# Kernel tuning notes

Measured on AMD Instinct MI355X. Metric: run time of the kernel, lower is better.

## Reference

```python
import jax, jax.numpy as jnp
import numpy as np
from jax import lax

H = 64
V = 32000
B = 32
T = 512


def setup_inputs() -> dict:
    key = jax.random.key(0)
    k1, k2, k3, k4 = jax.random.split(key, 4)
    # Parameters, constructed exactly as in SOHMM.__init__
    alpha_exp = jax.nn.softmax(jax.random.normal(k1, (H, H, H), dtype=jnp.float32), axis=2)
    beta = jax.nn.log_softmax(jax.random.normal(k2, (H, V), dtype=jnp.float32), axis=1)
    gamma = jax.nn.log_softmax(jax.random.normal(k3, (H, H), dtype=jnp.float32).reshape(-1)).reshape(H, H)
    input_ids = jax.random.randint(k4, (B, T), 0, V, dtype=jnp.int64)
    return {"alpha_exp": alpha_exp, "beta": beta, "gamma": gamma, "input_ids": input_ids}


def reference(alpha_exp, beta, gamma, input_ids):
    # input_ids: [B, T]
    h = alpha_exp.shape[0]
    b, t = input_ids.shape
    ids = input_ids.T  # [T, B]
    mask = (ids != -1)
    # emission log-probs per timestep: [T, H, B]; -1 padding tokens zeroed
    ip = jnp.transpose(beta[:, jnp.where(mask, ids, 0)], (1, 0, 2)) * mask[:, None, :].astype(beta.dtype)
    gamma_exp = jax.nn.softmax(gamma.reshape(-1)).reshape(gamma.shape)

    # t = T-1: y starts at zeros then adds emission
    y0 = jnp.zeros((h, h, b), dtype=beta.dtype) + ip[-1][None, :, :]

    def step(y, ip_t):
        y_max = y.max(axis=(0, 1), keepdims=True)            # [1,1,B]
        y_exp = jnp.exp(y - y_max)
        y = jnp.log(jnp.einsum('ijk,jkb->ijb', alpha_exp, y_exp)) + y_max
        y = y + ip_t[None, :, :]
        return y, y

    # loop t = T-2 .. 0 (reverse over remaining emissions)
    y_last, ys_rest = lax.scan(step, y0, ip[:-1][::-1])
    ys = jnp.concatenate([y0[None], ys_rest], axis=0)       # [T, H, H, B]

    y_max = y_last.max(axis=(0, 1))                          # [B]
    final = jnp.log(jnp.einsum('ij,ijb->b', gamma_exp, jnp.exp(y_last - y_max[None, None, :]))) + y_max
    return ys, final
```

## Files before the change

kernel.cpp:

```cpp
#include <hip/hip_runtime.h>
#include <cstdint>
#include <cstddef>

#define Hh 64
#define Vv 32000
#define Bb 32
#define Tt 512

typedef _Float16 half2_t __attribute__((ext_vector_type(2)));

#define IP_OFF    0ull
#define IP_SZ     ((size_t)Bb*Tt*Hh*4)
#define SL_OFF    (IP_OFF + IP_SZ)
#define SL_SZ     ((size_t)Bb*Tt*4)
#define U511_OFF  (SL_OFF + SL_SZ)
#define U511_SZ   ((size_t)Bb*Hh*Hh*4)
#define STAGE_OFF (U511_OFF + U511_SZ)
#define STAGE_SZ  ((size_t)Tt*Bb*Hh*Hh*2)

__device__ __forceinline__ float wave_max64(float v){
  #pragma unroll
  for (int off=32; off; off>>=1) v = fmaxf(v, __shfl_xor(v, off, 64));
  return v;
}

__device__ __forceinline__ half2_t pk16(float x, float y){
  return __builtin_bit_cast(half2_t, __builtin_amdgcn_cvt_pkrtz(x, y));
}

__global__ __launch_bounds__(256) void sohmm_ipfill(
    const float* __restrict__ beta, const int* __restrict__ ids,
    float* __restrict__ ipbuf)
{
  const int bid = blockIdx.x;
  const int b = bid >> 7, tq = bid & 127;
  const int t = tq*4 + (threadIdx.x >> 6);
  const int j = threadIdx.x & 63;
  const int id = ids[b*Tt + t];
  ipbuf[((size_t)b*Tt + t)*Hh + j] = beta[(size_t)j*Vv + id];
}

__global__ __launch_bounds__(512)
__attribute__((amdgpu_waves_per_eu(2, 2)))
void sohmm_scan(
    const float* __restrict__ alpha, const float* __restrict__ ipbuf,
    float* __restrict__ out, float* __restrict__ SL,
    float* __restrict__ u511, unsigned int* __restrict__ stage, int use_stage)
{
  const int b    = blockIdx.x;
  const int tid  = threadIdx.x;
  const int j    = tid >> 3;
  const int igrp = tid & 7;
  const int w    = tid >> 6;
  const int lane = tid & 63;
  const int i0   = igrp * 8;

  __shared__ char zb[2][64*128];
  __shared__ char aL[512*272];
  __shared__ float wred[2][8];

  half2_t areg[6][32];
  #pragma unroll
  for (int m=0; m<6; m++){
    const float4* ap = (const float4*)(alpha + (((size_t)(i0+m))*Hh + j)*Hh);
    #pragma unroll
    for (int q=0; q<16; q++){
      float4 v = ap[q];
      areg[m][2*q+0] = pk16(v.x, v.y);
      areg[m][2*q+1] = pk16(v.z, v.w);
    }
  }
  #pragma unroll
  for (int mm=0; mm<2; mm++){
    const float4* ap = (const float4*)(alpha + (((size_t)(i0+6+mm))*Hh + j)*Hh);
    #pragma unroll
    for (int q=0; q<8; q++){
      float4 v0 = ap[2*q], v1 = ap[2*q+1];
      uint4 u;
      u.x = __builtin_bit_cast(unsigned, __builtin_amdgcn_cvt_pkrtz(v0.x, v0.y));
      u.y = __builtin_bit_cast(unsigned, __builtin_amdgcn_cvt_pkrtz(v0.z, v0.w));
      u.z = __builtin_bit_cast(unsigned, __builtin_amdgcn_cvt_pkrtz(v1.x, v1.y));
      u.w = __builtin_bit_cast(unsigned, __builtin_amdgcn_cvt_pkrtz(v1.z, v1.w));
      *(uint4*)(aL + (size_t)tid*272 + mm*128 + q*16) = u;
    }
  }
  __syncthreads();

  const int kzj = ((j >> 3) ^ j) & 7;
  const int jc  = j >> 3;
  const int jo  = (j & 7) * 2;

  float L = 0.f;

  for (int s=0; s<Tt; s++){
    const int cs = s & 1, ps = cs ^ 1;
    const int t  = (Tt-1) - s;

    float ipv = ipbuf[((size_t)b*Tt + t)*Hh + j];

    float acc[8];
    #pragma unroll
    for (int m=0;m<8;m++) acc[m] = 0.f;

    if (s){
      const char* zrow = zb[ps] + j*128;
      const char* arow = aL + (size_t)tid*272;
      #pragma unroll
      for (int h=0; h<2; h++){
        unsigned zz[16];
        #pragma unroll
        for (int c=0; c<4; c++){
          uint4 zq = *(const uint4*)(zrow + (((h*4+c) ^ kzj) << 4));
          zz[4*c+0]=zq.x; zz[4*c+1]=zq.y; zz[4*c+2]=zq.z; zz[4*c+3]=zq.w;
        }
        #pragma unroll
        for (int m=0; m<6; m++){
          #pragma unroll
          for (int p=0; p<16; p++)
            acc[m] = __builtin_amdgcn_fdot2(areg[m][16*h+p],
                       __builtin_bit_cast(half2_t, zz[p]), acc[m], false);
        }
        #pragma unroll
        for (int mm=0; mm<2; mm++){
          unsigned aa[16];
          #pragma unroll
          for (int c=0; c<4; c++){
            uint4 aq = *(const uint4*)(arow + mm*128 + h*64 + c*16);
            aa[4*c+0]=aq.x; aa[4*c+1]=aq.y; aa[4*c+2]=aq.z; aa[4*c+3]=aq.w;
          }
          #pragma unroll
          for (int p=0; p<16; p++)
            acc[6+mm] = __builtin_amdgcn_fdot2(__builtin_bit_cast(half2_t, aa[p]),
                           __builtin_bit_cast(half2_t, zz[p]), acc[6+mm], false);
        }
      }
      float e = __expf(ipv);
      #pragma unroll
      for (int m=0;m<8;m++) acc[m] *= e;
    } else {
      float e = __expf(ipv);
      #pragma unroll
      for (int m=0;m<8;m++) acc[m] = e;
    }

    float vm = acc[0];
    #pragma unroll
    for (int m=1;m<8;m++) vm = fmaxf(vm, acc[m]);
    vm = wave_max64(vm);
    if (lane==0) wred[cs][w] = vm;

    if (s){
      float mu8 = wred[ps][0];
      #pragma unroll
      for (int q=1;q<8;q++) mu8 = fmaxf(mu8, wred[ps][q]);
      L += __logf(mu8);
    }
    if (tid==0) SL[(size_t)b*Tt + s] = L;

    if (use_stage){
      unsigned pk4[4];
      #pragma unroll
      for (int q=0;q<4;q++)
        pk4[q] = (__float_as_uint(acc[2*q]) >> 16) | (__float_as_uint(acc[2*q+1]) & 0xFFFF0000u);
      uint4 o; o.x=pk4[0]; o.y=pk4[1]; o.z=pk4[2]; o.w=pk4[3];
      *(uint4*)(stage + ((size_t)s*Bb + b)*2048 + (size_t)j*32 + igrp*4) = o;
    } else {
      #pragma unroll
      for (int m=0;m<8;m++)
        out[(((size_t)s*Hh + (i0+m))*Hh + j)*Bb + b] = __logf(acc[m]) + L;
    }
    if (s == Tt-1){
      float4* ud = (float4*)(u511 + (size_t)b*4096 + (size_t)j*64 + i0);
      #pragma unroll
      for (int q=0;q<2;q++){
        float4 o; o.x=acc[4*q]; o.y=acc[4*q+1]; o.z=acc[4*q+2]; o.w=acc[4*q+3];
        ud[q] = o;
      }
    }

    __syncthreads();

    float mu   = wred[cs][0];
    #pragma unroll
    for (int q=1;q<8;q++) mu = fmaxf(mu, wred[cs][q]);
    float rinv = 1.0f / mu;
    {
      #pragma unroll
      for (int m=0;m<8;m++){
        int i = i0 + m;
        int ck = (jc ^ igrp ^ m) & 7;
        _Float16 hv = (_Float16)fmaxf(acc[m]*rinv, 1e-7f);
        *(short*)(zb[cs] + i*128 + (ck<<4) + jo) = __builtin_bit_cast(short, hv);
      }
    }
    __syncthreads();
  }
}

__global__ __launch_bounds__(256) void sohmm_emit(
    const unsigned short* __restrict__ stage, const float* __restrict__ SL,
    float* __restrict__ out)
{
  const int s  = blockIdx.x >> 3;
  const int jb = blockIdx.x & 7;
  const int tid = threadIdx.x;

  __shared__ unsigned short T[32*514];
  __shared__ float Sl[32];

  if (tid < 32) Sl[tid] = SL[(size_t)tid*Tt + s];

  #pragma unroll 4
  for (int bb=0; bb<32; bb++){
    ushort2 v = ((const ushort2*)(stage + ((size_t)s*Bb + bb)*4096 + (size_t)jb*512))[tid];
    *(ushort2*)(&T[bb*514 + tid*2]) = v;
  }
  __syncthreads();

  const int bch = tid & 31;
  const int pg  = tid >> 5;
  #pragma unroll 4
  for (int r=0; r<64; r++){
    int p  = r*8 + pg;
    int jr = p >> 6;
    int i  = p & 63;
    unsigned short h = T[bch*514 + jr*64 + i];
    float u = __uint_as_float(((unsigned)h) << 16);
    out[(((size_t)s*Hh + i)*Hh + (jb*8 + jr))*Bb + bch] = __logf(u) + Sl[bch];
  }
}

__global__ __launch_bounds__(256) void sohmm_final(
    const float* __restrict__ gamma, const float* __restrict__ u511,
    const float* __restrict__ SL, float* __restrict__ out)
{
  const int b = blockIdx.x, tid = threadIdx.x;
  const int w = tid>>6, lane = tid&63;
  __shared__ float red[4], red2[4];

  float gm = -3.4e38f;
  #pragma unroll
  for (int q=0;q<16;q++) gm = fmaxf(gm, gamma[q*256+tid]);
  gm = wave_max64(gm);
  if (lane==0) red[w] = gm;
  __syncthreads();
  gm = fmaxf(fmaxf(red[0],red[1]), fmaxf(red[2],red[3]));
  __syncthreads();

  float se=0.f, dot=0.f;
  #pragma unroll
  for (int q=0;q<16;q++){
    int idx = q*256+tid;
    int ii = idx>>6, jj = idx&63;
    float gq = __expf(gamma[idx]-gm);
    se  += gq;
    dot += gq * u511[(size_t)b*4096 + (size_t)jj*64 + ii];
  }
  #pragma unroll
  for (int off=32; off; off>>=1){
    se  += __shfl_xor(se,  off, 64);
    dot += __shfl_xor(dot, off, 64);
  }
  if (lane==0){ red[w]=se; red2[w]=dot; }
  __syncthreads();
  if (tid==0){
    float ses  = red[0]+red[1]+red[2]+red[3];
    float dots = red2[0]+red2[1]+red2[2]+red2[3];
    out[(size_t)Tt*Hh*Hh*Bb + b] = __logf(dots/ses) + SL[(size_t)b*Tt + (Tt-1)];
  }
}

extern "C" void kernel_launch(void* const* d_in, const int* in_sizes, int n_in,
                              void* d_out, int out_size, void* d_ws, size_t ws_size,
                              hipStream_t stream)
{
  (void)in_sizes; (void)n_in; (void)out_size;
  const float* alpha = (const float*)d_in[0];
  const float* beta  = (const float*)d_in[1];
  const float* gamma = (const float*)d_in[2];
  const int*   ids   = (const int*)d_in[3];
  float* out = (float*)d_out;
  char*  ws  = (char*)d_ws;

  float*          ipbuf = (float*)(ws + IP_OFF);
  float*          SLp   = (float*)(ws + SL_OFF);
  float*          u511p = (float*)(ws + U511_OFF);
  unsigned int*   stage = (unsigned int*)(ws + STAGE_OFF);

  const int use_stage = (ws_size >= STAGE_OFF + STAGE_SZ) ? 1 : 0;

  hipLaunchKernelGGL(sohmm_ipfill, dim3(Bb*128), dim3(256), 0, stream, beta, ids, ipbuf);
  hipLaunchKernelGGL(sohmm_scan, dim3(Bb), dim3(512), 0, stream,
                     alpha, ipbuf, out, SLp, u511p, stage, use_stage);
  if (use_stage){
    hipLaunchKernelGGL(sohmm_emit, dim3(Tt*8), dim3(256), 0, stream,
                       (const unsigned short*)stage, SLp, out);
  }
  hipLaunchKernelGGL(sohmm_final, dim3(Bb), dim3(256), 0, stream,
                     gamma, u511p, SLp, out);
}
```

Measured before the change: 1.217 ms.

## Defer max renormalization by one step to drop a barrier per scan iteration

Each step's values are now rescaled by the previous step's block max and by a precomputed per-timestep emission max, which the ipfill kernel computes with a wave reduction. This removes the second __syncthreads and the in-step block-max reduction from every one of the 512 sequential scan steps. It also drops the waves_per_eu attribute. The risk is a weaker bound on fp16 range, since values are normalized by a one-step-stale max and can exceed 1 before conversion.

```diff
diff --git a/kernel.cpp b/kernel.cpp
--- a/kernel.cpp
+++ b/kernel.cpp
@@ -13,7 +13,9 @@
 #define IP_SZ     ((size_t)Bb*Tt*Hh*4)
 #define SL_OFF    (IP_OFF + IP_SZ)
 #define SL_SZ     ((size_t)Bb*Tt*4)
-#define U511_OFF  (SL_OFF + SL_SZ)
+#define DM_OFF    (SL_OFF + SL_SZ)
+#define DM_SZ     ((size_t)Bb*Tt*4)
+#define U511_OFF  (DM_OFF + DM_SZ)
 #define U511_SZ   ((size_t)Bb*Hh*Hh*4)
 #define STAGE_OFF (U511_OFF + U511_SZ)
 #define STAGE_SZ  ((size_t)Tt*Bb*Hh*Hh*2)
@@ -30,20 +32,23 @@
 
 __global__ __launch_bounds__(256) void sohmm_ipfill(
     const float* __restrict__ beta, const int* __restrict__ ids,
-    float* __restrict__ ipbuf)
+    float* __restrict__ ipbuf, float* __restrict__ dmax)
 {
   const int bid = blockIdx.x;
   const int b = bid >> 7, tq = bid & 127;
   const int t = tq*4 + (threadIdx.x >> 6);
   const int j = threadIdx.x & 63;
   const int id = ids[b*Tt + t];
-  ipbuf[((size_t)b*Tt + t)*Hh + j] = beta[(size_t)j*Vv + id];
+  float ip = beta[(size_t)j*Vv + id];
+  ipbuf[((size_t)b*Tt + t)*Hh + j] = ip;
+  float m = wave_max64(ip);
+  if (j == 0) dmax[b*Tt + t] = m;
 }
 
 __global__ __launch_bounds__(512)
-__attribute__((amdgpu_waves_per_eu(2, 2)))
 void sohmm_scan(
     const float* __restrict__ alpha, const float* __restrict__ ipbuf,
+    const float* __restrict__ dmax,
     float* __restrict__ out, float* __restrict__ SL,
     float* __restrict__ u511, unsigned int* __restrict__ stage, int use_stage)
 {
@@ -90,19 +95,30 @@
   const int jc  = j >> 3;
   const int jo  = (j & 7) * 2;
 
-  float L = 0.f;
+  float logC = 0.f;
 
   for (int s=0; s<Tt; s++){
     const int cs = s & 1, ps = cs ^ 1;
     const int t  = (Tt-1) - s;
 
     float ipv = ipbuf[((size_t)b*Tt + t)*Hh + j];
-
-    float acc[8];
-    #pragma unroll
-    for (int m=0;m<8;m++) acc[m] = 0.f;
+    float dmv = dmax[b*Tt + t];
+
+    float y[8];
 
     if (s){
+      uint4 w0 = *(const uint4*)(&wred[ps][0]);
+      uint4 w1 = *(const uint4*)(&wred[ps][4]);
+      float Mprev = fmaxf(
+        fmaxf(fmaxf(__uint_as_float(w0.x),__uint_as_float(w0.y)),
+              fmaxf(__uint_as_float(w0.z),__uint_as_float(w0.w))),
+        fmaxf(fmaxf(__uint_as_float(w1.x),__uint_as_float(w1.y)),
+              fmaxf(__uint_as_float(w1.z),__uint_as_float(w1.w))));
+
+      float acc[8];
+      #pragma unroll
+      for (int m=0;m<8;m++) acc[m] = 0.f;
+
       const char* zrow = zb[ps] + j*128;
       const char* arow = aL + (size_t)tid*272;
       #pragma unroll
@@ -134,65 +150,56 @@
                            __builtin_bit_cast(half2_t, zz[p]), acc[6+mm], false);
         }
       }
-      float e = __expf(ipv);
-      #pragma unroll
-      for (int m=0;m<8;m++) acc[m] *= e;
+      float scale = __expf(ipv - dmv) / Mprev;
+      #pragma unroll
+      for (int m=0;m<8;m++) y[m] = acc[m] * scale;
+      logC += __logf(Mprev) + dmv;
     } else {
-      float e = __expf(ipv);
-      #pragma unroll
-      for (int m=0;m<8;m++) acc[m] = e;
-    }
-
-    float vm = acc[0];
+      float e = __expf(ipv - dmv);
+      #pragma unroll
+      for (int m=0;m<8;m++) y[m] = e;
+      logC = dmv;
+    }
+
+    float vm = y[0];
     #pragma unroll
-    for (int m=1;m<8;m++) vm = fmaxf(vm, acc[m]);
+    for (int m=1;m<8;m++) vm = fmaxf(vm, y[m]);
     vm = wave_max64(vm);
     if (lane==0) wred[cs][w] = vm;
 
-    if (s){
-      float mu8 = wred[ps][0];
-      #pragma unroll
-      for (int q=1;q<8;q++) mu8 = fmaxf(mu8, wred[ps][q]);
-      L += __logf(mu8);
-    }
-    if (tid==0) SL[(size_t)b*Tt + s] = L;
+    if (tid==0) SL[(size_t)b*Tt + s] = logC;
 
     if (use_stage){
       unsigned pk4[4];
       #pragma unroll
       for (int q=0;q<4;q++)
-        pk4[q] = (__float_as_uint(acc[2*q]) >> 16) | (__float_as_uint(acc[2*q+1]) & 0xFFFF0000u);
+        pk4[q] = (__float_as_uint(y[2*q]) >> 16) | (__float_as_uint(y[2*q+1]) & 0xFFFF0000u);
       uint4 o; o.x=pk4[0]; o.y=pk4[1]; o.z=pk4[2]; o.w=pk4[3];
       *(uint4*)(stage + ((size_t)s*Bb + b)*2048 + (size_t)j*32 + igrp*4) = o;
     } else {
       #pragma unroll
       for (int m=0;m<8;m++)
-        out[(((size_t)s*Hh + (i0+m))*Hh + j)*Bb + b] = __logf(acc[m]) + L;
+        out[(((size_t)s*Hh + (i0+m))*Hh + j)*Bb + b] = __logf(y[m]) + logC;
     }
     if (s == Tt-1){
       float4* ud = (float4*)(u511 + (size_t)b*4096 + (size_t)j*64 + i0);
       #pragma unroll
       for (int q=0;q<2;q++){
-        float4 o; o.x=acc[4*q]; o.y=acc[4*q+1]; o.z=acc[4*q+2]; o.w=acc[4*q+3];
+        float4 o; o.x=y[4*q]; o.y=y[4*q+1]; o.z=y[4*q+2]; o.w=y[4*q+3];
         ud[q] = o;
       }
     }
 
-    __syncthreads();
-
-    float mu   = wred[cs][0];
-    #pragma unroll
-    for (int q=1;q<8;q++) mu = fmaxf(mu, wred[cs][q]);
-    float rinv = 1.0f / mu;
     {
       #pragma unroll
       for (int m=0;m<8;m++){
         int i = i0 + m;
         int ck = (jc ^ igrp ^ m) & 7;
-        _Float16 hv = (_Float16)fmaxf(acc[m]*rinv, 1e-7f);
+        _Float16 hv = (_Float16)fmaxf(y[m], 1e-7f);
         *(short*)(zb[cs] + i*128 + (ck<<4) + jo) = __builtin_bit_cast(short, hv);
       }
     }
+
     __syncthreads();
   }
 }
@@ -284,14 +291,16 @@
 
   float*          ipbuf = (float*)(ws + IP_OFF);
   float*          SLp   = (float*)(ws + SL_OFF);
+  float*          dmaxp = (float*)(ws + DM_OFF);
   float*          u511p = (float*)(ws + U511_OFF);
   unsigned int*   stage = (unsigned int*)(ws + STAGE_OFF);
 
   const int use_stage = (ws_size >= STAGE_OFF + STAGE_SZ) ? 1 : 0;
 
-  hipLaunchKernelGGL(sohmm_ipfill, dim3(Bb*128), dim3(256), 0, stream, beta, ids, ipbuf);
+  hipLaunchKernelGGL(sohmm_ipfill, dim3(Bb*128), dim3(256), 0, stream,
+                     beta, ids, ipbuf, dmaxp);
   hipLaunchKernelGGL(sohmm_scan, dim3(Bb), dim3(512), 0, stream,
-                     alpha, ipbuf, out, SLp, u511p, stage, use_stage);
+                     alpha, ipbuf, dmaxp, out, SLp, u511p, stage, use_stage);
   if (use_stage){
     hipLaunchKernelGGL(sohmm_emit, dim3(Tt*8), dim3(256), 0, stream,
                        (const unsigned short*)stage, SLp, out);
```

After: 1.171 ms. -3.7%, faster.
